# Kernel optimization log

Measured on AMD Instinct MI355X. Metric: run time of the kernel, lower is better.

Reference implementation:

```python
import jax, jax.numpy as jnp
import numpy as np

L = 8      # num_hidden_layers
J = 3      # num_gnn_layers
N = 2000   # num nodes (<=2000 so prune=False)
E = 32000  # num edges
R = 64     # num relations
HID = 1024 # hidden_dim
G = 128    # gnn_dim
H = 8      # num_gnn_heads
DH = G // H          # 16 per-head dim
P = 10               # pre_seq_len
KV = 8               # plm_num_kv_heads
OUT = HID // 32 * KV # out_ft_dim = 256
B = 16               # batch (h.shape[0])


def setup_inputs() -> dict:
    key = jax.random.key(0)
    ks = jax.random.split(key, 24)
    f = lambda k, s: (jax.random.normal(k, s, dtype=jnp.float32) * 0.05)
    ri = lambda k, s, hi: jax.random.randint(k, s, 0, hi, dtype=jnp.int32)
    return {
        'nft': f(ks[0], (L, N, HID)),
        'rft': f(ks[1], (L, R, HID)),
        'importances': jax.random.normal(ks[2], (N,), dtype=jnp.float32),
        'tg_w': f(ks[3], (L, HID, G)),
        'tg_b': f(ks[4], (L, G)),
        'path_w': f(ks[5], (L, J, 3 * G, G)),
        'path_b': f(ks[6], (L, J, G)),
        'attn1_w': f(ks[7], (L, J, G, H)),
        'attn2_p': f(ks[8], (L, J, H, DH)),
        'trans_w': f(ks[9], (L, G, 2 * OUT)),
        'trans_b': f(ks[10], (L, 2 * OUT)),
        'lamda': jnp.zeros((L - 1,), dtype=jnp.float32),
        'edge_src': ri(ks[11], (E,), N),
        'edge_dst': ri(ks[12], (E,), N),
        'edge_label': ri(ks[13], (E,), R),
        'h': ri(ks[14], (B,), N),
        't': ri(ks[15], (B,), N),
    }


def _gat(x, eft, src, dst, Wp, bp, Wa1, a2p):
    # x: [N, G], eft: [E, G]
    ns = x[src]                       # [E, G] gather src node feats
    ne = x[dst]                       # [E, G] gather dst node feats
    epaths = (jnp.concatenate([ns, eft, ne], axis=-1) @ Wp + bp)
    epaths = epaths.reshape(E, H, DH)           # per-edge multi-head features
    a1 = ns @ Wa1                               # [E, H]
    a2 = jnp.einsum('ehd,hd->eh', epaths, a2p)  # [E, H]
    a = jax.nn.leaky_relu(a1 + a2)              # slope 0.01, matches torch default
    # edge softmax grouped by destination node
    amax = jax.ops.segment_max(a, dst, num_segments=N)
    ex = jnp.exp(a - amax[dst])
    ssum = jax.ops.segment_sum(ex, dst, num_segments=N)
    attn = ex / ssum[dst]                       # [E, H]
    msg = epaths * attn[..., None]              # [E, H, DH]
    agg = jax.ops.segment_sum(msg, dst, num_segments=N)  # [N, H, DH]
    return jax.nn.relu(agg.reshape(N, G) + x)


def reference(nft, rft, importances, tg_w, tg_b, path_w, path_b, attn1_w,
              attn2_p, trans_w, trans_b, lamda, edge_src, edge_dst,
              edge_label, h, t):
    bsz = h.shape[0]
    # topk indices of node importances (prune=False path)
    _, imp_idx = jax.lax.top_k(importances, P)
    pkv = []
    for i in range(L):
        x = nft[i] @ tg_w[i] + tg_b[i]                       # [N, G]
        # linear-then-gather == gather-then-linear (same math, less traffic)
        rel = rft[i] @ tg_w[i] + tg_b[i]                     # [R, G]
        gnn_eft = rel[edge_label]                            # [E, G]
        for j in range(J):
            x = _gat(x, gnn_eft, edge_src, edge_dst,
                     path_w[i, j], path_b[i, j], attn1_w[i, j], attn2_p[i, j])
        past_x = x
        if i > 0:
            s = jax.nn.sigmoid(lamda[i - 1] / 0.1)
            x = s * x + (1.0 - s) * past_x   # past_x == x (as in source)
        prefix = x[imp_idx]                                  # [P, G]
        pk = jnp.tanh(prefix) @ trans_w[i] + trans_b[i]      # [P, 2*OUT]
        pk = jnp.broadcast_to(pk[None], (bsz, P, 2 * OUT))
        pk = pk.reshape(bsz, P, 2, KV, OUT // KV).transpose(2, 0, 3, 1, 4)
        pkv.append(pk)
    return jnp.stack(pkv)   # [L, 2, B, KV, P, OUT//KV]
```

## Files before the change

kernel.cpp:

```cpp
#include <hip/hip_runtime.h>
#include <hip/hip_bf16.h>
#include <math.h>

#define L_    8
#define J_    3
#define N_    2000
#define E_    32000
#define R_    64
#define HID_  1024
#define G_    128
#define H_    8
#define DH_   16
#define P_    10
#define KV_   8
#define OUT2_ 512
#define B_    16
#define ROWS_ 2064
#define CAP_  64

typedef float f32x4 __attribute__((ext_vector_type(4)));
typedef short s16x8 __attribute__((ext_vector_type(8)));

__device__ __forceinline__ void cvt_split1(float v, short& h, short& l) {
    unsigned u = __float_as_uint(v);
    h = (short)(u >> 16);
    float rem = v - __uint_as_float(u & 0xffff0000u);
    l = (short)(__float_as_uint(rem) >> 16);
}

__device__ __forceinline__ void cvt_split8(const float* v, s16x8& h, s16x8& l) {
    #pragma unroll
    for (int i = 0; i < 8; ++i) {
        unsigned u = __float_as_uint(v[i]);
        h[i] = (short)(u >> 16);
        float rem = v[i] - __uint_as_float(u & 0xffff0000u);
        l[i] = (short)(__float_as_uint(rem) >> 16);
    }
}

__device__ __forceinline__ void cvt_split8v(float4 a, float4 b, s16x8& h, s16x8& l) {
    short hh, ll;
    cvt_split1(a.x, hh, ll); h[0] = hh; l[0] = ll;
    cvt_split1(a.y, hh, ll); h[1] = hh; l[1] = ll;
    cvt_split1(a.z, hh, ll); h[2] = hh; l[2] = ll;
    cvt_split1(a.w, hh, ll); h[3] = hh; l[3] = ll;
    cvt_split1(b.x, hh, ll); h[4] = hh; l[4] = ll;
    cvt_split1(b.y, hh, ll); h[5] = hh; l[5] = ll;
    cvt_split1(b.z, hh, ll); h[6] = hh; l[6] = ll;
    cvt_split1(b.w, hh, ll); h[7] = hh; l[7] = ll;
}


__device__ __forceinline__ void place_body(int b, const int* __restrict__ dst,
                                           const int* __restrict__ src,
                                           const int* __restrict__ lab,
                                           int* __restrict__ cur,
                                           int2* __restrict__ sl) {
    int e = b * 256 + threadIdx.x;
    if (e < E_) {
        int n = dst[e];
        int slot = atomicAdd(&cur[n], 1);
        sl[n * CAP_ + slot] = make_int2(src[e], lab[e]);
    }
}

__device__ __forceinline__ void topk_body(const float* __restrict__ imp,
                                          int* __restrict__ idx_out) {
    __shared__ float sv[N_];
    __shared__ float rv[256];
    __shared__ int   ri[256];
    int t = threadIdx.x;
    for (int i = t; i < N_; i += 256) sv[i] = imp[i];
    __syncthreads();
    for (int k = 0; k < P_; ++k) {
        float bv = -INFINITY; int bi = N_;
        for (int i = t; i < N_; i += 256) {
            float v = sv[i];
            if (v > bv || (v == bv && i < bi)) { bv = v; bi = i; }
        }
        rv[t] = bv; ri[t] = bi;
        __syncthreads();
        for (int s = 128; s > 0; s >>= 1) {
            if (t < s) {
                float v = rv[t + s]; int i2 = ri[t + s];
                if (v > rv[t] || (v == rv[t] && i2 < ri[t])) { rv[t] = v; ri[t] = i2; }
            }
            __syncthreads();
        }
        if (t == 0) { idx_out[k] = ri[0]; sv[ri[0]] = -INFINITY; }
        __syncthreads();
    }
}

__device__ __forceinline__ void wsplitB_body(int layer, int gst,
                                             const float* __restrict__ tg_w,
                                             short* __restrict__ WpkB) {
    int tid = threadIdx.x;
    int col = tid & 127, khalf = tid >> 7;
    const float* src = tg_w + ((size_t)layer * HID_ + gst * 32 + khalf * 16) * G_ + col;
    short* dh = WpkB + ((size_t)(layer * 32 + gst) * 2 + 0) * 4096 + col * 32 + khalf * 16;
    short* dl = WpkB + ((size_t)(layer * 32 + gst) * 2 + 1) * 4096 + col * 32 + khalf * 16;
    #pragma unroll
    for (int kk = 0; kk < 16; ++kk) {
        short h, l;
        cvt_split1(src[(size_t)kk * G_], h, l);
        dh[kk] = h; dl[kk] = l;
    }
}

__device__ __forceinline__ void psplit_body(int l, int j, int halfc, int st,
                                            const float* __restrict__ path_w,
                                            short* __restrict__ Ppk) {
    int lj = l * J_ + j;
    int tid = threadIdx.x;
    int col = tid & 127, khalf = tid >> 7;
    int c0 = halfc ? 256 : 0;
    const float* src = path_w + (size_t)lj * 384 * G_ + (size_t)(c0 + st * 32 + khalf * 16) * G_ + col;
    size_t base = (((size_t)lj * 2 + halfc) * 4 + st) * 2;
    short* dh = Ppk + (base + 0) * 4096 + tid * 16;
    short* dl = Ppk + (base + 1) * 4096 + tid * 16;
    #pragma unroll
    for (int kk = 0; kk < 16; ++kk) {
        short h, l;
        cvt_split1(src[(size_t)kk * G_], h, l);
        dh[kk] = h; dl[kk] = l;
    }
}

__device__ __forceinline__ void prep_body(int combo, int q,
                                          const float* __restrict__ path_w,
                                          const float* __restrict__ path_b,
                                          const float* __restrict__ attn1_w,
                                          const float* __restrict__ attn2_p,
                                          float* __restrict__ wPR,
                                          short* __restrict__ PPk,
                                          float* __restrict__ bA) {
    int j = combo / L_;
    int l = combo % L_;
    int t = threadIdx.x;
    size_t wb = (size_t)((l * J_ + j) * 384) * G_;
    size_t ob = (size_t)(j * L_ + l);
    const float* a2 = attn2_p + (size_t)(l * J_ + j) * G_;
    short* pph = PPk + (ob * 2 + 0) * 2048;
    short* ppl = PPk + (ob * 2 + 1) * 2048;
    int i = q * 256 + t;
    {
        int k = i >> 3, h = i & 7;
        const float* a2h = a2 + h * DH_;
        float s1 = 0.f, s2 = 0.f, s3 = 0.f;
        for (int d = 0; d < DH_; ++d) {
            float av = a2h[d];
            int c = h * DH_ + d;
            s1 += path_w[wb + (size_t)k * G_ + c] * av;
            s3 += path_w[wb + (size_t)(128 + k) * G_ + c] * av;
            s2 += path_w[wb + (size_t)(256 + k) * G_ + c] * av;
        }
        s1 += attn1_w[((size_t)(l * J_ + j) * G_ + k) * H_ + h];
        short h1, l1, h2, l2;
        cvt_split1(s1, h1, l1);
        cvt_split1(s2, h2, l2);
        pph[h * 128 + k] = h1;       ppl[h * 128 + k] = l1;
        pph[(8 + h) * 128 + k] = h2; ppl[(8 + h) * 128 + k] = l2;
        wPR[ob * H_ * G_ + h * G_ + k] = s3;
    }
    if (q == 0 && t < H_) {
        float s = 0.f;
        const float* a2h = a2 + t * DH_;
        const float* pb = path_b + (size_t)(l * J_ + j) * G_ + t * DH_;
        for (int d = 0; d < DH_; ++d) s += pb[d] * a2h[d];
        bA[ob * H_ + t] = s;
    }
}

__global__ __launch_bounds__(256) void k_pre1(
    const int* __restrict__ edst, const int* __restrict__ esrc,
    const int* __restrict__ elab, const float* __restrict__ imp,
    const float* __restrict__ tg_w, const float* __restrict__ path_w,
    const float* __restrict__ path_b, const float* __restrict__ attn1_w,
    const float* __restrict__ attn2_p,
    int* __restrict__ cur, int2* __restrict__ csr_sl, int* __restrict__ imp_idx,
    short* __restrict__ WpkB, short* __restrict__ Ppk,
    float* __restrict__ wPR, short* __restrict__ PPk, float* __restrict__ bA) {
    int b = blockIdx.x;
    if (b < 125) { place_body(b, edst, esrc, elab, cur, csr_sl); return; }
    if (b == 125) { topk_body(imp, imp_idx); return; }
    if (b < 382) {
        int w = b - 126;
        wsplitB_body((w + 1) & 7, w >> 3, tg_w, WpkB);
        return;
    }
    if (b < 574) {
        int w = b - 382;
        int l = (w + 6) & 7;
        int m = w >> 3;
        int j = m % 3;
        int hs = m / 3;
        psplit_body(l, j, hs >> 2, hs & 3, path_w, Ppk);
        return;
    }
    {
        int w = b - 574;
        prep_body(w >> 2, w & 3, path_w, path_b, attn1_w, attn2_p, wPR, PPk, bA);
    }
}

__global__ __launch_bounds__(128, 2) void k_pre3(
    const float* __restrict__ nft, const float* __restrict__ rft,
    const short* __restrict__ WpkB, const float* __restrict__ tg_b,
    float* __restrict__ x0, float* __restrict__ rel) {
    __shared__ alignas(16) float Abf[3 * 1024];
    const int b2 = blockIdx.x;
    const int layer = b2 & 7;
    const int rg = b2 >> 3;
    const int row0 = rg * 32;
    const int tid = threadIdx.x;
    const int lane = tid & 63, wv = tid >> 6;
    const int lr = lane & 15, kg = lane >> 4;

    char* ldsb = (char*)Abf;

    const float* gsrc0;
    const float* gsrc1;
    {
        int swz = ((lane & 7) ^ (lane >> 3)) << 2;
        int rl0 = wv * 16 + (lane >> 3);
        int rl1 = rl0 + 8;
        int g0 = row0 + rl0; if (g0 > ROWS_ - 1) g0 = ROWS_ - 1;
        int g1 = row0 + rl1; if (g1 > ROWS_ - 1) g1 = ROWS_ - 1;
        gsrc0 = ((g0 < N_) ? nft + ((size_t)layer * N_ + g0) * HID_
                           : rft + ((size_t)layer * R_ + (g0 - N_)) * HID_) + swz;
        gsrc1 = ((g1 < N_) ? nft + ((size_t)layer * N_ + g1) * HID_
                           : rft + ((size_t)layer * R_ + (g1 - N_)) * HID_) + swz;
    }
    const short* WB = WpkB + (size_t)layer * 262144 + ((wv * 64 + lr) * 32 + kg * 8);

    f32x4 zero = {0.f, 0.f, 0.f, 0.f};
    f32x4 acc[2][4];
    #pragma unroll
    for (int i = 0; i < 2; ++i)
        #pragma unroll
        for (int n = 0; n < 4; ++n) acc[i][n] = zero;

    s16x8 bs[2][4][2];

#define LDA(WR, GST) do { \
    char* lb_ = ldsb + (WR) * 4096 + wv * 2048; \
    __builtin_amdgcn_global_load_lds( \
        (const __attribute__((address_space(1))) void*)(gsrc0 + (GST) * 32), \
        (__attribute__((address_space(3))) void*)(lb_), 16, 0, 0); \
    __builtin_amdgcn_global_load_lds( \
        (const __attribute__((address_space(1))) void*)(gsrc1 + (GST) * 32), \
        (__attribute__((address_space(3))) void*)(lb_ + 1024), 16, 0, 0); \
} while (0)

#define LDB(SL, GST) do { \
    const short* bp_ = WB + (size_t)(GST) * 8192; \
    _Pragma("unroll") \
    for (int n_ = 0; n_ < 4; ++n_) { \
        bs[SL][n_][0] = *(const s16x8*)(bp_ + n_ * 512); \
        bs[SL][n_][1] = *(const s16x8*)(bp_ + n_ * 512 + 4096); \
    } \
} while (0)

#define COMP(CUR, SL) do { \
    const int o1_ = (kg * 32) ^ ((lr & 7) << 4); \
    _Pragma("unroll") \
    for (int mf_ = 0; mf_ < 2; ++mf_) { \
        const char* ap_ = ldsb + (CUR) * 4096 + (mf_ * 16 + lr) * 128; \
        float4 av0_ = *(const float4*)(ap_ + o1_); \
        float4 av1_ = *(const float4*)(ap_ + (o1_ ^ 16)); \
        s16x8 ah_, al_; \
        cvt_split8v(av0_, av1_, ah_, al_); \
        _Pragma("unroll") \
        for (int n_ = 0; n_ < 4; ++n_) { \
            acc[mf_][n_] = __builtin_amdgcn_mfma_f32_16x16x32_bf16(ah_, bs[SL][n_][0], acc[mf_][n_], 0, 0, 0); \
            acc[mf_][n_] = __builtin_amdgcn_mfma_f32_16x16x32_bf16(ah_, bs[SL][n_][1], acc[mf_][n_], 0, 0, 0); \
            acc[mf_][n_] = __builtin_amdgcn_mfma_f32_16x16x32_bf16(al_, bs[SL][n_][0], acc[mf_][n_], 0, 0, 0); \
        } \
    } \
} while (0)

#define TGITER(ST, CUR, WR, SL, SLN) do { \
    LDB(SLN, (ST) + 1); \
    LDA(WR, (ST) + 2); \
    asm volatile("s_waitcnt vmcnt(12)" ::: "memory"); \
    __builtin_amdgcn_s_barrier(); \
    COMP(CUR, SL); \
    __builtin_amdgcn_s_barrier(); \
} while (0)

    LDA(0, 0);
    LDA(1, 1);
    LDB(0, 0);
    for (int st = 0; st < 30; st += 6) {
        TGITER(st + 0, 0, 2, 0, 1);
        TGITER(st + 1, 1, 0, 1, 0);
        TGITER(st + 2, 2, 1, 0, 1);
        TGITER(st + 3, 0, 2, 1, 0);
        TGITER(st + 4, 1, 0, 0, 1);
        TGITER(st + 5, 2, 1, 1, 0);
    }
    LDB(1, 31);
    asm volatile("s_waitcnt vmcnt(10)" ::: "memory");
    __builtin_amdgcn_s_barrier();
    COMP(0, 0);
    asm volatile("s_waitcnt vmcnt(0)" ::: "memory");
    __builtin_amdgcn_s_barrier();
    COMP(1, 1);
#undef LDA
#undef LDB
#undef COMP
#undef TGITER

    #pragma unroll
    for (int n = 0; n < 4; ++n) {
        int col = wv * 64 + n * 16 + lr;
        float bias = tg_b[layer * G_ + col];
        #pragma unroll
        for (int mf = 0; mf < 2; ++mf) {
            #pragma unroll
            for (int rgi = 0; rgi < 4; ++rgi) {
                int row = row0 + mf * 16 + kg * 4 + rgi;
                if (row >= ROWS_) continue;
                float v = acc[mf][n][rgi] + bias;
                if (row < N_) x0[((size_t)layer * N_ + row) * G_ + col] = v;
                else          rel[((size_t)layer * R_ + (row - N_)) * G_ + col] = v;
            }
        }
    }
}

__device__ __forceinline__ void rel_body(
    int blk, char* pool,
    const float* __restrict__ rel, const float* __restrict__ path_w,
    const float* __restrict__ wPR, float* __restrict__ Rl, float* __restrict__ PR) {
    float (*At)[132] = (float(*)[132])pool;
    float (*Wt)[132] = (float(*)[132])(pool + 16896);
    const int tid = threadIdx.x;
    const int halfb = blk & 1;
    const int t2 = blk >> 1;
    const int l = t2 % L_;
    const int j = t2 / L_;
    const int row0 = halfb * 32;
    const size_t ob = (size_t)(j * L_ + l);
    {
        int ar = tid >> 3, aq2 = tid & 7;
        const float* asrc = rel + ((size_t)l * R_ + row0 + ar) * G_ + aq2 * 16;
        float4 a0 = ((const float4*)asrc)[0], a1 = ((const float4*)asrc)[1];
        float4 a2 = ((const float4*)asrc)[2], a3 = ((const float4*)asrc)[3];
        *(float4*)&At[ar][aq2 * 16]      = a0;
        *(float4*)&At[ar][aq2 * 16 + 4]  = a1;
        *(float4*)&At[ar][aq2 * 16 + 8]  = a2;
        *(float4*)&At[ar][aq2 * 16 + 12] = a3;
    }
    const size_t wb = (size_t)((l * J_ + j) * 384) * G_;
    const int wrow = tid >> 3, wq = tid & 7;
    float4 rW0, rW1, rW2, rW3;
    auto loadW = [&](int kt) {
        const float* src = path_w + wb + (size_t)(128 + kt * 32 + wrow) * G_ + wq * 16;
        rW0 = ((const float4*)src)[0]; rW1 = ((const float4*)src)[1];
        rW2 = ((const float4*)src)[2]; rW3 = ((const float4*)src)[3];
    };
    const int tr = tid >> 4;
    const int tc = tid & 15;
    float4 acc[2][2];
    acc[0][0] = make_float4(0, 0, 0, 0); acc[0][1] = make_float4(0, 0, 0, 0);
    acc[1][0] = make_float4(0, 0, 0, 0); acc[1][1] = make_float4(0, 0, 0, 0);
    loadW(0);
    for (int wt = 0; wt < 4; ++wt) {
        __syncthreads();
        *(float4*)&Wt[wrow][wq * 16]      = rW0;
        *(float4*)&Wt[wrow][wq * 16 + 4]  = rW1;
        *(float4*)&Wt[wrow][wq * 16 + 8]  = rW2;
        *(float4*)&Wt[wrow][wq * 16 + 12] = rW3;
        __syncthreads();
        if (wt + 1 < 4) loadW(wt + 1);
        #pragma unroll
        for (int kk = 0; kk < 32; ++kk) {
            float4 w0 = *(const float4*)&Wt[kk][tc * 4];
            float4 w1 = *(const float4*)&Wt[kk][64 + tc * 4];
            float a0 = At[tr * 2][wt * 32 + kk];
            float a1 = At[tr * 2 + 1][wt * 32 + kk];
            acc[0][0].x += a0 * w0.x; acc[0][0].y += a0 * w0.y;
            acc[0][0].z += a0 * w0.z; acc[0][0].w += a0 * w0.w;
            acc[0][1].x += a0 * w1.x; acc[0][1].y += a0 * w1.y;
            acc[0][1].z += a0 * w1.z; acc[0][1].w += a0 * w1.w;
            acc[1][0].x += a1 * w0.x; acc[1][0].y += a1 * w0.y;
            acc[1][0].z += a1 * w0.z; acc[1][0].w += a1 * w0.w;
            acc[1][1].x += a1 * w1.x; acc[1][1].y += a1 * w1.y;
            acc[1][1].z += a1 * w1.z; acc[1][1].w += a1 * w1.w;
        }
    }
    #pragma unroll
    for (int r2 = 0; r2 < 2; ++r2) {
        int row = row0 + tr * 2 + r2;
        float* dst = Rl + (ob * R_ + row) * G_;
        *(float4*)(dst + tc * 4) = acc[r2][0];
        *(float4*)(dst + 64 + tc * 4) = acc[r2][1];
    }
    {
        int prow = tid >> 3, ph = tid & 7;
        const float* wp = wPR + (ob * H_ + ph) * G_;
        float s = 0.f;
        for (int k = 0; k < G_; ++k) s += At[prow][k] * wp[k];
        PR[(ob * R_ + row0 + prow) * H_ + ph] = s;
    }
}

__global__ __launch_bounds__(256) void k_proj2(
    const float* __restrict__ xcur, const short* __restrict__ Ppk,
    const short* __restrict__ PPkj, const float* __restrict__ bAj,
    const float* __restrict__ path_b, int j,
    float* __restrict__ Xs, float* __restrict__ XdB,
    float* __restrict__ PS, float* __restrict__ PDb,
    const float* __restrict__ rel, const float* __restrict__ path_w,
    const float* __restrict__ wPR, float* __restrict__ Rl, float* __restrict__ PR) {
    __shared__ alignas(16) char POOL[39424];
    if (blockIdx.x >= 512) { rel_body(blockIdx.x - 512, POOL, rel, path_w, wPR, Rl, PR); return; }
    short (*Ah)[40]   = (short(*)[40])(POOL);
    short (*Al)[40]   = (short(*)[40])(POOL + 5120);
    short (*Wh)[40]   = (short(*)[40])(POOL + 10240);
    short (*Wl)[40]   = (short(*)[40])(POOL + 20480);
    short (*PPh)[136] = (short(*)[136])(POOL + 30720);
    short (*PPl)[136] = (short(*)[136])(POOL + 35072);
    const int tid = threadIdx.x;
    const int layer = blockIdx.x & 7;
    const int rest = blockIdx.x >> 3;
    const int halfb = rest & 1;
    const int rg = rest >> 1;
    const int row0 = rg * 64;

    const int arow = tid >> 2, aq = tid & 3;
    int gra = row0 + arow; if (gra >= N_) gra = N_ - 1;
    const float* asrc = xcur + ((size_t)layer * N_ + gra) * G_;
    const int wcol = tid & 127, wkh = tid >> 7;

    const int lane = tid & 63, wv = tid >> 6;
    const int lr = lane & 15, lk = (lane >> 4) * 8;

    if (!halfb) {
        int col = tid >> 4, koff = (tid & 15) * 8;
        s16x8 vh = *(const s16x8*)(PPkj + ((size_t)layer * 2 + 0) * 2048 + tid * 8);
        s16x8 vl = *(const s16x8*)(PPkj + ((size_t)layer * 2 + 1) * 2048 + tid * 8);
        *(s16x8*)&PPh[col][koff] = vh;
        *(s16x8*)&PPl[col][koff] = vl;
    }

    f32x4 zero = {0.f, 0.f, 0.f, 0.f};
    f32x4 acc[4][2];
    f32x4 acc_pp[2];
    #pragma unroll
    for (int i = 0; i < 4; ++i) { acc[i][0] = zero; acc[i][1] = zero; }
    acc_pp[0] = zero; acc_pp[1] = zero;

    float aa[8];
    s16x8 wh0, wh1, wl0, wl1;
    const size_t pbase = (((size_t)(layer * J_ + j) * 2 + halfb) * 4) * 2;
    auto ldG = [&](int st) {
        int kk0 = st * 32;
        *(float4*)&aa[0] = *(const float4*)(asrc + kk0 + aq * 8);
        *(float4*)&aa[4] = *(const float4*)(asrc + kk0 + aq * 8 + 4);
        const s16x8* ph = (const s16x8*)(Ppk + (pbase + (size_t)st * 2 + 0) * 4096 + tid * 16);
        const s16x8* pl = (const s16x8*)(Ppk + (pbase + (size_t)st * 2 + 1) * 4096 + tid * 16);
        wh0 = ph[0]; wh1 = ph[1];
        wl0 = pl[0]; wl1 = pl[1];
    };
    ldG(0);
    for (int st = 0; st < 4; ++st) {
        __syncthreads();
        {
            s16x8 h, l; cvt_split8(aa, h, l);
            *(s16x8*)&Ah[arow][aq * 8] = h;
            *(s16x8*)&Al[arow][aq * 8] = l;
            *(s16x8*)&Wh[wcol][wkh * 16]     = wh0;
            *(s16x8*)&Wh[wcol][wkh * 16 + 8] = wh1;
            *(s16x8*)&Wl[wcol][wkh * 16]     = wl0;
            *(s16x8*)&Wl[wcol][wkh * 16 + 8] = wl1;
        }
        __syncthreads();
        if (st + 1 < 4) ldG(st + 1);
        s16x8 bh[2], bl[2];
        #pragma unroll
        for (int c = 0; c < 2; ++c) {
            int col = wv * 32 + c * 16 + lr;
            bh[c] = *(s16x8*)&Wh[col][lk];
            bl[c] = *(s16x8*)&Wl[col][lk];
        }
        s16x8 ppb_h, ppb_l;
        if (!halfb) {
            ppb_h = *(s16x8*)&PPh[lr][st * 32 + lk];
            ppb_l = *(s16x8*)&PPl[lr][st * 32 + lk];
        }
        #pragma unroll
        for (int mf = 0; mf < 4; ++mf) {
            s16x8 ah = *(s16x8*)&Ah[mf * 16 + lr][lk];
            s16x8 al = *(s16x8*)&Al[mf * 16 + lr][lk];
            #pragma unroll
            for (int c = 0; c < 2; ++c) {
                acc[mf][c] = __builtin_amdgcn_mfma_f32_16x16x32_bf16(ah, bh[c], acc[mf][c], 0, 0, 0);
                acc[mf][c] = __builtin_amdgcn_mfma_f32_16x16x32_bf16(ah, bl[c], acc[mf][c], 0, 0, 0);
                acc[mf][c] = __builtin_amdgcn_mfma_f32_16x16x32_bf16(al, bh[c], acc[mf][c], 0, 0, 0);
            }
            if (!halfb && (mf >> 1) == wv) {
                int i = mf & 1;
                acc_pp[i] = __builtin_amdgcn_mfma_f32_16x16x32_bf16(ah, ppb_h, acc_pp[i], 0, 0, 0);
                acc_pp[i] = __builtin_amdgcn_mfma_f32_16x16x32_bf16(ah, ppb_l, acc_pp[i], 0, 0, 0);
                acc_pp[i] = __builtin_amdgcn_mfma_f32_16x16x32_bf16(al, ppb_h, acc_pp[i], 0, 0, 0);
            }
        }
    }
    const float* pb = path_b + (size_t)(layer * J_ + j) * G_;
    float* outp = halfb ? XdB : Xs;
    const int rbase = (lane >> 4) * 4;
    #pragma unroll
    for (int mf = 0; mf < 4; ++mf) {
        #pragma unroll
        for (int c = 0; c < 2; ++c) {
            int col = wv * 32 + c * 16 + lr;
            float bias = halfb ? pb[col] : 0.f;
            #pragma unroll
            for (int rgi = 0; rgi < 4; ++rgi) {
                int row = row0 + mf * 16 + rbase + rgi;
                if (row < N_) outp[((size_t)layer * N_ + row) * G_ + col] = acc[mf][c][rgi] + bias;
            }
        }
    }
    if (!halfb) {
        #pragma unroll
        for (int i = 0; i < 2; ++i) {
            int mf = wv * 2 + i;
            #pragma unroll
            for (int rgi = 0; rgi < 4; ++rgi) {
                int row = row0 + mf * 16 + rbase + rgi;
                if (row >= N_) continue;
                float val = acc_pp[i][rgi];
                if (lr < 8) PS[((size_t)layer * N_ + row) * H_ + lr] = val;
                else        PDb[((size_t)layer * N_ + row) * H_ + (lr - 8)] = val + bAj[layer * H_ + (lr - 8)];
            }
        }
    }
}

__global__ __launch_bounds__(256) void k_node(
    const float* __restrict__ xcur, const float* __restrict__ Xs,
    const float* __restrict__ XdB, const float* __restrict__ Rlj,
    const float* __restrict__ PS, const float* __restrict__ PDb,
    const float* __restrict__ PRj,
    const int* __restrict__ cnt, const int2* __restrict__ csr_sl,
    float* __restrict__ xnext) {
    int l = blockIdx.x & 7;
    int n = (blockIdx.x >> 3) * 4 + (threadIdx.x >> 6);
    int lane = threadIdx.x & 63;
    int o0 = n * CAP_, o1 = o0 + cnt[n];
    const float* xr = xcur + ((size_t)l * N_ + n) * G_;
    float xv0 = xr[lane], xv1 = xr[lane + 64];
    float xd0 = XdB[((size_t)l * N_ + n) * G_ + lane];
    float xd1 = XdB[((size_t)l * N_ + n) * G_ + lane + 64];
    float out0, out1;
    if (o1 == o0) {
        out0 = fmaxf(xv0, 0.f);
        out1 = fmaxf(xv1, 0.f);
    } else {
        const int h0 = lane >> 4, h1 = h0 + 4;
        const float pd0 = PDb[((size_t)l * N_ + n) * H_ + h0];
        const float pd1 = PDb[((size_t)l * N_ + n) * H_ + h1];
        const float* PSl = PS + (size_t)l * N_ * H_;
        const float* PRl = PRj + (size_t)l * R_ * H_;
        const float* Xsl = Xs + (size_t)l * N_ * G_;
        const float* Rll = Rlj + (size_t)l * R_ * G_;
        float acc0 = 0.f, acc1 = 0.f, sum0 = 0.f, sum1 = 0.f;
        #pragma unroll 2
        for (int k = o0; k < o1; ++k) {
            int2 sl = csr_sl[k];
            float lg0 = PSl[sl.x * H_ + h0] + PRl[sl.y * H_ + h0] + pd0;
            float lg1 = PSl[sl.x * H_ + h1] + PRl[sl.y * H_ + h1] + pd1;
            lg0 = (lg0 >= 0.f) ? lg0 : 0.01f * lg0;
            lg1 = (lg1 >= 0.f) ? lg1 : 0.01f * lg1;
            float e0 = __expf(lg0), e1 = __expf(lg1);
            float v0 = Xsl[(size_t)sl.x * G_ + lane]      + Rll[(size_t)sl.y * G_ + lane];
            float v1 = Xsl[(size_t)sl.x * G_ + lane + 64] + Rll[(size_t)sl.y * G_ + lane + 64];
            acc0 += e0 * v0; sum0 += e0;
            acc1 += e1 * v1; sum1 += e1;
        }
        out0 = fmaxf(acc0 / sum0 + xd0 + xv0, 0.f);
        out1 = fmaxf(acc1 / sum1 + xd1 + xv1, 0.f);
    }
    float* dst = xnext + ((size_t)l * N_ + n) * G_;
    dst[lane] = out0;
    dst[lane + 64] = out1;
}

__global__ __launch_bounds__(256) void k_out(
    const float* __restrict__ xfin, const int* __restrict__ imp_idx,
    const float* __restrict__ trans_w, const float* __restrict__ trans_b,
    float* __restrict__ out) {
    int blk = blockIdx.x;
    int layer = blk / (P_ * 2);
    int rem = blk % (P_ * 2);
    int p = rem >> 1;
    int half = rem & 1;
    __shared__ float th[G_];
    int t = threadIdx.x;
    int row = imp_idx[p];
    if (t < G_) th[t] = tanhf(xfin[((size_t)layer * N_ + row) * G_ + t]);
    __syncthreads();
    int c = half * 256 + t;
    float s = trans_b[layer * OUT2_ + c];
    const float* W = trans_w + (size_t)layer * G_ * OUT2_ + c;
    #pragma unroll 4
    for (int k = 0; k < G_; ++k) s += th[k] * W[(size_t)k * OUT2_];
    int c2 = c >> 8, kv = (c >> 5) & 7, oo = c & 31;
    for (int b = 0; b < B_; ++b) {
        out[(((((size_t)layer * 2 + c2) * B_ + b) * KV_ + kv) * P_ + p) * 32 + oo] = s;
    }
}

extern "C" void kernel_launch(void* const* d_in, const int* in_sizes, int n_in,
                              void* d_out, int out_size, void* d_ws, size_t ws_size,
                              hipStream_t stream) {
    const float* nft     = (const float*)d_in[0];
    const float* rft     = (const float*)d_in[1];
    const float* imp     = (const float*)d_in[2];
    const float* tg_w    = (const float*)d_in[3];
    const float* tg_b    = (const float*)d_in[4];
    const float* path_w  = (const float*)d_in[5];
    const float* path_b  = (const float*)d_in[6];
    const float* attn1_w = (const float*)d_in[7];
    const float* attn2_p = (const float*)d_in[8];
    const float* trans_w = (const float*)d_in[9];
    const float* trans_b = (const float*)d_in[10];
    const int* esrc = (const int*)d_in[12];
    const int* edst = (const int*)d_in[13];
    const int* elab = (const int*)d_in[14];
    float* out = (float*)d_out;

    char* w = (char*)d_ws;
    size_t off = 0;
    auto alloc = [&](size_t bytes) {
        void* p = w + off;
        off += (bytes + 255) & ~(size_t)255;
        return p;
    };
    float* x0      = (float*)alloc((size_t)L_ * N_ * G_ * 4);
    float* x1      = (float*)alloc((size_t)L_ * N_ * G_ * 4);
    float* rel     = (float*)alloc((size_t)L_ * R_ * G_ * 4);
    float* Xs      = (float*)alloc((size_t)L_ * N_ * G_ * 4);
    float* XdB     = (float*)alloc((size_t)L_ * N_ * G_ * 4);
    float* Rl      = (float*)alloc((size_t)J_ * L_ * R_ * G_ * 4);
    float* PS      = (float*)alloc((size_t)L_ * N_ * H_ * 4);
    float* PDb     = (float*)alloc((size_t)L_ * N_ * H_ * 4);
    float* PR      = (float*)alloc((size_t)J_ * L_ * R_ * H_ * 4);
    float* wPR     = (float*)alloc((size_t)J_ * L_ * H_ * G_ * 4);
    float* bA      = (float*)alloc((size_t)J_ * L_ * H_ * 4);
    short* Wpk     = (short*)alloc((size_t)L_ * 32 * 2 * 4096 * 2);
    short* Ppk     = (short*)alloc((size_t)L_ * J_ * 2 * 4 * 2 * 4096 * 2);
    short* PPk     = (short*)alloc((size_t)J_ * L_ * 2 * 2048 * 2);
    int*   cur     = (int*)alloc(N_ * 4);
    int2*  csr_sl  = (int2*)alloc((size_t)N_ * CAP_ * 8);
    int*   imp_idx = (int*)alloc(P_ * 4);

    hipMemsetAsync(cur, 0, N_ * 4, stream);

    k_pre1<<<125 + 1 + 256 + 192 + 96, 256, 0, stream>>>(
        edst, esrc, elab, imp, tg_w, path_w, path_b, attn1_w, attn2_p,
        cur, csr_sl, imp_idx, Wpk, Ppk, wPR, PPk, bA);
    k_pre3<<<520, 128, 0, stream>>>(nft, rft, Wpk, tg_b, x0, rel);

    float* xc = x0;
    float* xn = x1;
    for (int j = 0; j < J_; ++j) {
        int grid = (j == 0) ? (512 + J_ * L_ * 2) : 512;
        k_proj2<<<grid, 256, 0, stream>>>(
            xc, Ppk, PPk + (size_t)j * L_ * 2 * 2048, bA + (size_t)j * L_ * H_,
            path_b, j, Xs, XdB, PS, PDb,
            rel, path_w, wPR, Rl, PR);
        k_node<<<L_ * 500, 256, 0, stream>>>(
            xc, Xs, XdB, Rl + (size_t)j * L_ * R_ * G_, PS, PDb,
            PR + (size_t)j * L_ * R_ * H_,
            cur, csr_sl, xn);
        float* tmp = xc; xc = xn; xn = tmp;
    }
    k_out<<<L_ * P_ * 2, 256, 0, stream>>>(xc, imp_idx, trans_w, trans_b, out);
}
```

Before: 203.4 us.

## Split preprocessing so independent prep work runs alongside the tg_w projection kernel

The tg_w weight split-and-pack moves into a small first kernel, which also zeroes the CSR counters in place of a separate memset. The edge CSR placement, top-k, path_w split and attention prep blocks are appended as extra blocks of the 128-thread projection kernel, with their bodies rewritten for 128 threads and a shared LDS pool. The aim is to cut one launch plus the memset and let independent prep work fill the machine alongside the GEMM blocks. The catch is that the GEMM kernel's launch bounds now cover heterogeneous blocks, and the projection must wait for the full tg_w split before starting.

```diff
diff --git a/kernel.cpp b/kernel.cpp
--- a/kernel.cpp
+++ b/kernel.cpp
@@ -56,7 +56,7 @@
                                            const int* __restrict__ lab,
                                            int* __restrict__ cur,
                                            int2* __restrict__ sl) {
-    int e = b * 256 + threadIdx.x;
+    int e = b * 128 + threadIdx.x;
     if (e < E_) {
         int n = dst[e];
         int slot = atomicAdd(&cur[n], 1);
@@ -65,22 +65,22 @@
 }
 
 __device__ __forceinline__ void topk_body(const float* __restrict__ imp,
-                                          int* __restrict__ idx_out) {
-    __shared__ float sv[N_];
-    __shared__ float rv[256];
-    __shared__ int   ri[256];
+                                          int* __restrict__ idx_out, char* pool) {
+    float* sv = (float*)pool;
+    float* rv = (float*)(pool + 8192);
+    int*   ri = (int*)(pool + 8704);
     int t = threadIdx.x;
-    for (int i = t; i < N_; i += 256) sv[i] = imp[i];
+    for (int i = t; i < N_; i += 128) sv[i] = imp[i];
     __syncthreads();
     for (int k = 0; k < P_; ++k) {
         float bv = -INFINITY; int bi = N_;
-        for (int i = t; i < N_; i += 256) {
+        for (int i = t; i < N_; i += 128) {
             float v = sv[i];
             if (v > bv || (v == bv && i < bi)) { bv = v; bi = i; }
         }
         rv[t] = bv; ri[t] = bi;
         __syncthreads();
-        for (int s = 128; s > 0; s >>= 1) {
+        for (int s = 64; s > 0; s >>= 1) {
             if (t < s) {
                 float v = rv[t + s]; int i2 = ri[t + s];
                 if (v > rv[t] || (v == rv[t] && i2 < ri[t])) { rv[t] = v; ri[t] = i2; }
@@ -92,38 +92,25 @@
     }
 }
 
-__device__ __forceinline__ void wsplitB_body(int layer, int gst,
-                                             const float* __restrict__ tg_w,
-                                             short* __restrict__ WpkB) {
-    int tid = threadIdx.x;
-    int col = tid & 127, khalf = tid >> 7;
-    const float* src = tg_w + ((size_t)layer * HID_ + gst * 32 + khalf * 16) * G_ + col;
-    short* dh = WpkB + ((size_t)(layer * 32 + gst) * 2 + 0) * 4096 + col * 32 + khalf * 16;
-    short* dl = WpkB + ((size_t)(layer * 32 + gst) * 2 + 1) * 4096 + col * 32 + khalf * 16;
-    #pragma unroll
-    for (int kk = 0; kk < 16; ++kk) {
-        short h, l;
-        cvt_split1(src[(size_t)kk * G_], h, l);
-        dh[kk] = h; dl[kk] = l;
-    }
-}
-
 __device__ __forceinline__ void psplit_body(int l, int j, int halfc, int st,
                                             const float* __restrict__ path_w,
                                             short* __restrict__ Ppk) {
     int lj = l * J_ + j;
-    int tid = threadIdx.x;
-    int col = tid & 127, khalf = tid >> 7;
+    int col = threadIdx.x;
     int c0 = halfc ? 256 : 0;
-    const float* src = path_w + (size_t)lj * 384 * G_ + (size_t)(c0 + st * 32 + khalf * 16) * G_ + col;
     size_t base = (((size_t)lj * 2 + halfc) * 4 + st) * 2;
-    short* dh = Ppk + (base + 0) * 4096 + tid * 16;
-    short* dl = Ppk + (base + 1) * 4096 + tid * 16;
-    #pragma unroll
-    for (int kk = 0; kk < 16; ++kk) {
-        short h, l;
-        cvt_split1(src[(size_t)kk * G_], h, l);
-        dh[kk] = h; dl[kk] = l;
+    #pragma unroll
+    for (int khalf = 0; khalf < 2; ++khalf) {
+        const float* src = path_w + (size_t)lj * 384 * G_
+                         + (size_t)(c0 + st * 32 + khalf * 16) * G_ + col;
+        short* dh = Ppk + (base + 0) * 4096 + (khalf * 128 + col) * 16;
+        short* dl = Ppk + (base + 1) * 4096 + (khalf * 128 + col) * 16;
+        #pragma unroll
+        for (int kk = 0; kk < 16; ++kk) {
+            short h, l2;
+            cvt_split1(src[(size_t)kk * G_], h, l2);
+            dh[kk] = h; dl[kk] = l2;
+        }
     }
 }
 
@@ -143,8 +130,9 @@
     const float* a2 = attn2_p + (size_t)(l * J_ + j) * G_;
     short* pph = PPk + (ob * 2 + 0) * 2048;
     short* ppl = PPk + (ob * 2 + 1) * 2048;
-    int i = q * 256 + t;
-    {
+    #pragma unroll
+    for (int h2 = 0; h2 < 2; ++h2) {
+        int i = q * 256 + h2 * 128 + t;
         int k = i >> 3, h = i & 7;
         const float* a2h = a2 + h * DH_;
         float s1 = 0.f, s2 = 0.f, s3 = 0.f;
@@ -156,11 +144,11 @@
             s2 += path_w[wb + (size_t)(256 + k) * G_ + c] * av;
         }
         s1 += attn1_w[((size_t)(l * J_ + j) * G_ + k) * H_ + h];
-        short h1, l1, h2, l2;
+        short h1, l1, hh2, l2;
         cvt_split1(s1, h1, l1);
-        cvt_split1(s2, h2, l2);
-        pph[h * 128 + k] = h1;       ppl[h * 128 + k] = l1;
-        pph[(8 + h) * 128 + k] = h2; ppl[(8 + h) * 128 + k] = l2;
+        cvt_split1(s2, hh2, l2);
+        pph[h * 128 + k] = h1;        ppl[h * 128 + k] = l1;
+        pph[(8 + h) * 128 + k] = hh2; ppl[(8 + h) * 128 + k] = l2;
         wPR[ob * H_ * G_ + h * G_ + k] = s3;
     }
     if (q == 0 && t < H_) {
@@ -172,44 +160,60 @@
     }
 }
 
-__global__ __launch_bounds__(256) void k_pre1(
-    const int* __restrict__ edst, const int* __restrict__ esrc,
-    const int* __restrict__ elab, const float* __restrict__ imp,
-    const float* __restrict__ tg_w, const float* __restrict__ path_w,
-    const float* __restrict__ path_b, const float* __restrict__ attn1_w,
-    const float* __restrict__ attn2_p,
-    int* __restrict__ cur, int2* __restrict__ csr_sl, int* __restrict__ imp_idx,
-    short* __restrict__ WpkB, short* __restrict__ Ppk,
-    float* __restrict__ wPR, short* __restrict__ PPk, float* __restrict__ bA) {
+__global__ __launch_bounds__(256) void k_pre0(
+    const float* __restrict__ tg_w, short* __restrict__ WpkB,
+    int* __restrict__ cur) {
     int b = blockIdx.x;
-    if (b < 125) { place_body(b, edst, esrc, elab, cur, csr_sl); return; }
-    if (b == 125) { topk_body(imp, imp_idx); return; }
-    if (b < 382) {
-        int w = b - 126;
-        wsplitB_body((w + 1) & 7, w >> 3, tg_w, WpkB);
+    if (b == 256) {
+        for (int i = threadIdx.x; i < N_; i += 256) cur[i] = 0;
         return;
     }
-    if (b < 574) {
-        int w = b - 382;
-        int l = (w + 6) & 7;
-        int m = w >> 3;
-        int j = m % 3;
-        int hs = m / 3;
-        psplit_body(l, j, hs >> 2, hs & 3, path_w, Ppk);
-        return;
-    }
-    {
-        int w = b - 574;
-        prep_body(w >> 2, w & 3, path_w, path_b, attn1_w, attn2_p, wPR, PPk, bA);
+    int layer = b & 7, gst = b >> 3;
+    int tid = threadIdx.x;
+    int col = tid & 127, khalf = tid >> 7;
+    const float* src = tg_w + ((size_t)layer * HID_ + gst * 32 + khalf * 16) * G_ + col;
+    short* dh = WpkB + ((size_t)(layer * 32 + gst) * 2 + 0) * 4096 + col * 32 + khalf * 16;
+    short* dl = WpkB + ((size_t)(layer * 32 + gst) * 2 + 1) * 4096 + col * 32 + khalf * 16;
+    #pragma unroll
+    for (int kk = 0; kk < 16; ++kk) {
+        short h, l;
+        cvt_split1(src[(size_t)kk * G_], h, l);
+        dh[kk] = h; dl[kk] = l;
     }
 }
 
 __global__ __launch_bounds__(128, 2) void k_pre3(
     const float* __restrict__ nft, const float* __restrict__ rft,
     const short* __restrict__ WpkB, const float* __restrict__ tg_b,
-    float* __restrict__ x0, float* __restrict__ rel) {
-    __shared__ alignas(16) float Abf[3 * 1024];
-    const int b2 = blockIdx.x;
+    float* __restrict__ x0, float* __restrict__ rel,
+    const int* __restrict__ edst, const int* __restrict__ esrc,
+    const int* __restrict__ elab, const float* __restrict__ imp,
+    const float* __restrict__ path_w, const float* __restrict__ path_b,
+    const float* __restrict__ attn1_w, const float* __restrict__ attn2_p,
+    int* __restrict__ cur, int2* __restrict__ csr_sl, int* __restrict__ imp_idx,
+    short* __restrict__ Ppk, float* __restrict__ wPR,
+    short* __restrict__ PPk, float* __restrict__ bA) {
+    __shared__ alignas(16) char POOL3[12288];
+    int b = blockIdx.x;
+    if (b >= 520) {
+        int w = b - 520;
+        if (w < 250) { place_body(w, edst, esrc, elab, cur, csr_sl); return; }
+        if (w == 250) { topk_body(imp, imp_idx, POOL3); return; }
+        if (w < 443) {
+            int v = w - 251;
+            int l = v & 7, m = v >> 3;
+            int j = m % 3, hs = m / 3;
+            psplit_body(l, j, hs >> 2, hs & 3, path_w, Ppk);
+            return;
+        }
+        {
+            int v = w - 443;
+            prep_body(v >> 2, v & 3, path_w, path_b, attn1_w, attn2_p, wPR, PPk, bA);
+            return;
+        }
+    }
+
+    const int b2 = b;
     const int layer = b2 & 7;
     const int rg = b2 >> 3;
     const int row0 = rg * 32;
@@ -217,7 +221,7 @@
     const int lane = tid & 63, wv = tid >> 6;
     const int lr = lane & 15, kg = lane >> 4;
 
-    char* ldsb = (char*)Abf;
+    char* ldsb = POOL3;
 
     const float* gsrc0;
     const float* gsrc1;
@@ -659,12 +663,11 @@
     int2*  csr_sl  = (int2*)alloc((size_t)N_ * CAP_ * 8);
     int*   imp_idx = (int*)alloc(P_ * 4);
 
-    hipMemsetAsync(cur, 0, N_ * 4, stream);
-
-    k_pre1<<<125 + 1 + 256 + 192 + 96, 256, 0, stream>>>(
-        edst, esrc, elab, imp, tg_w, path_w, path_b, attn1_w, attn2_p,
-        cur, csr_sl, imp_idx, Wpk, Ppk, wPR, PPk, bA);
-    k_pre3<<<520, 128, 0, stream>>>(nft, rft, Wpk, tg_b, x0, rel);
+    k_pre0<<<257, 256, 0, stream>>>(tg_w, Wpk, cur);
+    k_pre3<<<520 + 250 + 1 + 192 + 96, 128, 0, stream>>>(
+        nft, rft, Wpk, tg_b, x0, rel,
+        edst, esrc, elab, imp, path_w, path_b, attn1_w, attn2_p,
+        cur, csr_sl, imp_idx, Ppk, wPR, PPk, bA);
 
     float* xc = x0;
     float* xn = x1;
```

Result: faster. 182.5 us (-10.2%).
